# Kernel tuning notes

Hardware: AMD Instinct MI355X
Metric: run time of the kernel (lower is better)

Reference implementation:

```python
import jax, jax.numpy as jnp
import numpy as np

B, T, C, H, D = 2, 2048, 768, 12, 64
ATTN_MULT = 0.125  # 1/sqrt(head_dim)


def setup_inputs() -> dict:
    key = jax.random.key(0)
    k0, k1, k2 = jax.random.split(key, 3)
    x = jax.random.normal(k0, (B, T, C), jnp.float32)
    w_attn = jax.random.normal(k1, (3 * H * D, C), jnp.float32) * 0.02
    b_attn = jnp.zeros((3 * H * D,), jnp.float32)
    w_proj = jax.random.normal(k2, (C, H * D), jnp.float32) * 0.02
    b_proj = jnp.zeros((C,), jnp.float32)
    return {"x": x, "w_attn": w_attn, "b_attn": b_attn, "w_proj": w_proj, "b_proj": b_proj}


def reference(x, w_attn, b_attn, w_proj, b_proj):
    Bx, Tx, Cx = x.shape
    # fused qkv projection (torch nn.Linear: x @ W^T + b)
    qkv = x @ w_attn.T + b_attn                      # [B,T,3*H*D]
    q, k, v = jnp.split(qkv, 3, axis=2)
    def to_heads(t):
        return t.reshape(Bx, Tx, H, D).transpose(0, 2, 1, 3)  # [B,H,T,D]
    q, k, v = to_heads(q), to_heads(k), to_heads(v)
    att = jnp.einsum('bhqd,bhkd->bhqk', q, k) * ATTN_MULT     # [B,H,T,T]

    causal = jnp.tril(jnp.ones((Tx, Tx), dtype=bool))
    # selection scores from head 0 (selective attention)
    S = jax.nn.relu(att[:, 0])                                # [B,T,T]
    # prevent_from_masking_myself: zero diagonal; protect_bos_token: zero key col 0
    smask = causal & ~jnp.eye(Tx, dtype=bool)
    smask = smask.at[:, 0].set(False)
    S = jnp.where(smask, S, 0.0)
    # exclusive cumulative sum over the query dim: F[i,j] = sum_{i'<i} S[i',j]
    Fmask = jnp.cumsum(S, axis=-2) - S                        # [B,T,T]
    att = att - Fmask[:, None]                                # broadcast over heads

    att = jnp.where(causal, att, -jnp.inf)
    p = jax.nn.softmax(att, axis=-1)                          # [B,H,T,T]
    y = jnp.einsum('bhqk,bhkd->bhqd', p, v)                   # [B,H,T,D]
    y = y.transpose(0, 2, 1, 3).reshape(Bx, Tx, H * D)
    return y @ w_proj.T + b_proj
```

## Files before the change

### kernel.cpp

```cpp
#include <hip/hip_runtime.h>
#include <hip/hip_bf16.h>

#define BB 2
#define TT 2048
#define CC 768
#define HH 12
#define DD 64
#define NQKV 2304
#define MTOT (BB*TT)
#define CH 32
#define NCH (TT/CH)

typedef __bf16 bf16x8 __attribute__((ext_vector_type(8)));
typedef __bf16 bf16x4 __attribute__((ext_vector_type(4)));
typedef float  f32x4  __attribute__((ext_vector_type(4)));

__device__ __forceinline__ f32x4 mfma16(bf16x8 a, bf16x8 b, f32x4 c) {
    return __builtin_amdgcn_mfma_f32_16x16x32_bf16(a, b, c, 0, 0, 0);
}

__device__ __forceinline__ void load_lds16(const void* g, void* l) {
    __builtin_amdgcn_global_load_lds(
        (const __attribute__((address_space(1))) void*)g,
        (__attribute__((address_space(3))) void*)l, 16, 0, 0);
}

__global__ __launch_bounds__(256) void cvt_bf16_kernel(
    const float* __restrict__ x, const float* __restrict__ wa, const float* __restrict__ wp,
    __bf16* __restrict__ xb, __bf16* __restrict__ wab, __bf16* __restrict__ wpb)
{
    const long NX = (long)MTOT * CC;
    const long NWA = (long)NQKV * CC;
    long idx = ((long)blockIdx.x * 256 + threadIdx.x) * 4;
    const float* src; __bf16* dst; long off;
    if (idx < NX)            { src = x;  dst = xb;  off = idx; }
    else if (idx < NX + NWA) { src = wa; dst = wab; off = idx - NX; }
    else                     { src = wp; dst = wpb; off = idx - NX - NWA; }
    float4 v = *(const float4*)(src + off);
    bf16x4 o;
    o[0] = (__bf16)v.x; o[1] = (__bf16)v.y; o[2] = (__bf16)v.z; o[3] = (__bf16)v.w;
    *(bf16x4*)(dst + off) = o;
}

template<int EPI>
__global__ __launch_bounds__(256, 2) void gemm_nt_kernel(
    const __bf16* __restrict__ A, const __bf16* __restrict__ Bw,
    const float* __restrict__ bias,
    __bf16* __restrict__ oBF, float* __restrict__ oF32, int K)
{
    __shared__ __align__(16) __bf16 As[128 * 32];
    __shared__ __align__(16) __bf16 Bs[128 * 32];
    const int tid = threadIdx.x;
    const int m0 = blockIdx.y * 128, n0 = blockIdx.x * 128;
    const int w = tid >> 6, lane = tid & 63, quad = lane >> 4, l16 = lane & 15;
    const int wm = (w >> 1) * 64, wn = (w & 1) * 64;
    const int grow = w * 16 + (lane >> 2);
    const int gcol = (lane & 3) * 8;
    __bf16* AsW = As + w * 512;
    __bf16* BsW = Bs + w * 512;

    f32x4 acc[4][4] = {};

    for (int kt = 0; kt < K; kt += 32) {
        __syncthreads();
        load_lds16(A  + (long)(m0 + grow) * K + kt + gcol,      AsW);
        load_lds16(A  + (long)(m0 + grow + 64) * K + kt + gcol, AsW + 2048);
        load_lds16(Bw + (long)(n0 + grow) * K + kt + gcol,      BsW);
        load_lds16(Bw + (long)(n0 + grow + 64) * K + kt + gcol, BsW + 2048);
        __syncthreads();

        bf16x8 af[4], bfr[4];
#pragma unroll
        for (int g = 0; g < 4; g++)  af[g]  = *(const bf16x8*)(As + (wm + g * 16 + l16) * 32 + quad * 8);
#pragma unroll
        for (int jb = 0; jb < 4; jb++) bfr[jb] = *(const bf16x8*)(Bs + (wn + jb * 16 + l16) * 32 + quad * 8);
#pragma unroll
        for (int g = 0; g < 4; g++)
#pragma unroll
            for (int jb = 0; jb < 4; jb++)
                acc[g][jb] = mfma16(af[g], bfr[jb], acc[g][jb]);
    }

    const int ldc = (EPI == 0) ? NQKV : CC;
#pragma unroll
    for (int jb = 0; jb < 4; jb++) {
        const int n = n0 + wn + jb * 16 + l16;
        const float bv = bias[n];
#pragma unroll
        for (int g = 0; g < 4; g++) {
#pragma unroll
            for (int r = 0; r < 4; r++) {
                const int m = m0 + wm + g * 16 + quad * 4 + r;
                const float v = acc[g][jb][r] + bv;
                if (EPI == 0) oBF[(long)m * ldc + n] = (__bf16)v;
                else          oF32[(long)m * ldc + n] = v;
            }
        }
    }
}

__global__ __launch_bounds__(256) void transpose_v_kernel(
    const __bf16* __restrict__ qkv, __bf16* __restrict__ vT)
{
    __shared__ __bf16 Tl[64][72];
    const int tt = blockIdx.x, h = blockIdx.y, b = blockIdx.z;
    const int tid = threadIdx.x;
    const int r8 = tid >> 3, c8 = (tid & 7) * 8;
    const __bf16* src = qkv + (long)(b * TT + tt * 64) * NQKV + 1536 + h * 64;
#pragma unroll
    for (int p = 0; p < 2; p++) {
        const int row = p * 32 + r8;
        bf16x8 v = *(const bf16x8*)(src + (long)row * NQKV + c8);
#pragma unroll
        for (int e = 0; e < 8; e++) Tl[c8 + e][row] = v[e];
    }
    __syncthreads();
    __bf16* dst = vT + ((long)(b * HH + h) << 6) * TT + tt * 64;
#pragma unroll
    for (int p = 0; p < 2; p++) {
        const int d = p * 32 + r8;
        *(bf16x8*)(dst + (long)d * TT + c8) = *(const bf16x8*)(&Tl[d][c8]);
    }
}

__global__ __launch_bounds__(256) void sgemm_kernel(
    const __bf16* __restrict__ qkv, __bf16* __restrict__ S, float* __restrict__ csum)
{
    const int tj = blockIdx.x, ti = blockIdx.y, b = blockIdx.z;
    if (tj > ti) return;
    const int w = threadIdx.x >> 6, lane = threadIdx.x & 63, quad = lane >> 4, l16 = lane & 15;
    const int i0 = ti * 64 + w * 16;
    const int chunk = ti * 2 + (w >> 1);

    const __bf16* qp = qkv + (long)(b * TT + i0 + l16) * NQKV + quad * 8;
    bf16x8 a0 = *(const bf16x8*)qp, a1 = *(const bf16x8*)(qp + 32);
    const __bf16* kbase = qkv + (long)(b * TT) * NQKV + 768;

#pragma unroll
    for (int jb = 0; jb < 4; jb++) {
        const __bf16* kp = kbase + (long)(tj * 64 + jb * 16 + l16) * NQKV + quad * 8;
        bf16x8 b0 = *(const bf16x8*)kp, b1 = *(const bf16x8*)(kp + 32);
        f32x4 acc = {};
        acc = mfma16(a0, b0, acc);
        acc = mfma16(a1, b1, acc);
        const int j = tj * 64 + jb * 16 + l16;
        float colsum = 0.0f;
#pragma unroll
        for (int r = 0; r < 4; r++) {
            const int i = i0 + quad * 4 + r;
            float v = fmaxf(acc[r] * 0.125f, 0.0f);
            v = (j >= 1 && j < i) ? v : 0.0f;
            S[((long)b * TT + i) * TT + j] = (__bf16)v;
            colsum += v;
        }
        colsum += __shfl_xor(colsum, 16);
        colsum += __shfl_xor(colsum, 32);
        if (quad == 0)
            atomicAdd(&csum[((long)b * NCH + chunk) * TT + j], colsum);
    }
}

__global__ __launch_bounds__(256) void scan_write_kernel(
    const __bf16* __restrict__ S, const float* __restrict__ csum, __bf16* __restrict__ Fo)
{
    const int chunk = blockIdx.y, b = blockIdx.z;
    const int ib = chunk * CH;
    const int j0 = blockIdx.x * 256;
    if (j0 >= ib + CH) return;
    const int j = j0 + threadIdx.x;
    float off = 0.0f;
    for (int c = 0; c < chunk; c++) off += csum[((long)b * NCH + c) * TT + j];
    const __bf16* ps = S  + ((long)b * TT + ib) * TT + j;
    __bf16*       pf = Fo + ((long)b * TT + ib) * TT + j;
#pragma unroll
    for (int ii = 0; ii < CH; ii++) {
        float v = ((ib + ii) > j) ? (float)ps[(long)ii * TT] : 0.0f;
        pf[(long)ii * TT] = (__bf16)off;
        off += v;
    }
}

__global__ __launch_bounds__(128, 2) void flash_kernel(
    const __bf16* __restrict__ qkv, const __bf16* __restrict__ vT,
    const __bf16* __restrict__ F, __bf16* __restrict__ y)
{
    __shared__ __align__(16) __bf16 Ks[2][64 * 64];
    __shared__ __align__(16) __bf16 Vs[2][64 * 64];
    __shared__ __align__(16) __bf16 Pls[2][16 * 72];
    const int gid = blockIdx.x;
    const int xs = gid & 7, s = gid >> 3;
    const int gi = xs + ((s >> 5) << 3);
    const int bid = s & 31;
    const int h = gi % 12, b = gi / 12;
    const int w = threadIdx.x >> 6, lane = threadIdx.x & 63, quad = lane >> 4, l16 = lane & 15;
    const int rl = lane >> 3;
    const int cs8 = ((lane & 7) ^ rl) * 8;
    const int sw0 = ((quad)     ^ (l16 & 7)) * 8;
    const int sw1 = ((quad + 4) ^ (l16 & 7)) * 8;
    __bf16* Pl = &Pls[w][0];
    const __bf16* kb = qkv + (long)(b * TT) * NQKV + 768 + h * 64;
    const __bf16* vb = vT + ((long)(b * HH + h) << 6) * TT;
    const __bf16* Fbase = F + (long)b * TT * TT;

    const int qt0 = bid, qt1 = 63 - bid;
    const int n0 = (qt0 >> 1) + 1, n1 = (qt1 >> 1) + 1;
    const int N = n0 + n1;

    int i0 = qt0 * 32 + w * 16;
    const __bf16* qp = qkv + (long)(b * TT + i0 + l16) * NQKV + h * 64 + quad * 8;
    bf16x8 aq0 = *(const bf16x8*)qp;
    bf16x8 aq1 = *(const bf16x8*)(qp + 32);

    f32x4 O[4] = {};
    float lr[4] = {0.0f, 0.0f, 0.0f, 0.0f};
    __bf16 Fn[4][4];

    {
        __bf16* KsW = Ks[0] + w * 2048;
        __bf16* VsW = Vs[0] + w * 2048;
#pragma unroll
        for (int t = 0; t < 4; t++)
            load_lds16(kb + (long)(w * 32 + t * 8 + rl) * NQKV + cs8, KsW + t * 512);
#pragma unroll
        for (int t = 0; t < 4; t++)
            load_lds16(vb + (long)(w * 32 + t * 8 + rl) * TT + cs8, VsW + t * 512);
        const __bf16* Fb = Fbase + (long)i0 * TT;
#pragma unroll
        for (int jh = 0; jh < 4; jh++)
#pragma unroll
            for (int r = 0; r < 4; r++)
                Fn[jh][r] = Fb[(long)(quad * 4 + r) * TT + jh * 16 + l16];
    }

    for (int it = 0; it < N; it++) {
        const int ph = (it >= n0);
        const int jt = (it - (ph ? n0 : 0)) << 6;
        const int qt = ph ? qt1 : qt0;
        const int jtend = (qt >> 1) << 6;

        __syncthreads();

        __bf16 Fc[4][4];
#pragma unroll
        for (int jh = 0; jh < 4; jh++)
#pragma unroll
            for (int r = 0; r < 4; r++)
                Fc[jh][r] = Fn[jh][r];

        if (it + 1 < N) {
            const int ph2 = (it + 1 >= n0);
            const int jt2 = ((it + 1) - (ph2 ? n0 : 0)) << 6;
            __bf16* KsW = Ks[(it + 1) & 1] + w * 2048;
            __bf16* VsW = Vs[(it + 1) & 1] + w * 2048;
#pragma unroll
            for (int t = 0; t < 4; t++)
                load_lds16(kb + (long)(jt2 + w * 32 + t * 8 + rl) * NQKV + cs8, KsW + t * 512);
#pragma unroll
            for (int t = 0; t < 4; t++)
                load_lds16(vb + (long)(w * 32 + t * 8 + rl) * TT + jt2 + cs8, VsW + t * 512);
            const int i0n = (ph2 ? qt1 : qt0) * 32 + w * 16;
            const __bf16* Fb2 = Fbase + (long)i0n * TT;
#pragma unroll
            for (int jh = 0; jh < 4; jh++)
#pragma unroll
                for (int r = 0; r < 4; r++)
                    Fn[jh][r] = Fb2[(long)(quad * 4 + r) * TT + jt2 + jh * 16 + l16];
        }
        __builtin_amdgcn_sched_barrier(0);

        const __bf16* Kc = Ks[it & 1];
        const __bf16* Vc = Vs[it & 1];
        float sc[4][4];
#pragma unroll
        for (int jh = 0; jh < 4; jh++) {
            const int jr = jh * 16 + l16;
            const bf16x8 kc0 = *(const bf16x8*)(Kc + (jr << 6) + sw0);
            const bf16x8 kc1 = *(const bf16x8*)(Kc + (jr << 6) + sw1);
            f32x4 acc = {};
            acc = mfma16(aq0, kc0, acc);
            acc = mfma16(aq1, kc1, acc);
#pragma unroll
            for (int r = 0; r < 4; r++) sc[jh][r] = acc[r];
        }
        if (jt == jtend) {
#pragma unroll
            for (int jh = 0; jh < 4; jh++) {
                const int j = jt + jh * 16 + l16;
#pragma unroll
                for (int r = 0; r < 4; r++) {
                    const int i = i0 + quad * 4 + r;
                    float v = fmaf(sc[jh][r], 0.125f, -(float)Fc[jh][r]);
                    v = (j <= i) ? v : -35.0f;
                    const float p = __expf(v);
                    sc[jh][r] = p;
                    lr[r] += p;
                }
            }
        } else {
#pragma unroll
            for (int jh = 0; jh < 4; jh++) {
#pragma unroll
                for (int r = 0; r < 4; r++) {
                    float v = fmaf(sc[jh][r], 0.125f, -(float)Fc[jh][r]);
                    const float p = __expf(v);
                    sc[jh][r] = p;
                    lr[r] += p;
                }
            }
        }
#pragma unroll
        for (int r = 0; r < 4; r++) {
            const int il = quad * 4 + r;
#pragma unroll
            for (int jh = 0; jh < 4; jh++)
                Pl[il * 72 + jh * 16 + l16] = (__bf16)sc[jh][r];
        }
        const bf16x8 ap0 = *(const bf16x8*)(Pl + l16 * 72 + quad * 8);
        const bf16x8 ap1 = *(const bf16x8*)(Pl + l16 * 72 + 32 + quad * 8);
#pragma unroll
        for (int db = 0; db < 4; db++) {
            const bf16x8 vv0 = *(const bf16x8*)(Vc + ((db * 16 + l16) << 6) + sw0);
            const bf16x8 vv1 = *(const bf16x8*)(Vc + ((db * 16 + l16) << 6) + sw1);
            O[db] = mfma16(ap0, vv0, O[db]);
            O[db] = mfma16(ap1, vv1, O[db]);
        }
        if (jt == jtend) {
            float inv[4];
#pragma unroll
            for (int r = 0; r < 4; r++) {
                float s2 = lr[r];
#pragma unroll
                for (int off = 8; off >= 1; off >>= 1) s2 += __shfl_xor(s2, off, 16);
                inv[r] = 1.0f / s2;
            }
#pragma unroll
            for (int db = 0; db < 4; db++) {
#pragma unroll
                for (int r = 0; r < 4; r++) {
                    const int i = i0 + quad * 4 + r;
                    y[((long)(b * TT + i)) * (HH * DD) + h * 64 + db * 16 + l16] = (__bf16)(O[db][r] * inv[r]);
                }
            }
#pragma unroll
            for (int db = 0; db < 4; db++) { O[db][0] = 0.f; O[db][1] = 0.f; O[db][2] = 0.f; O[db][3] = 0.f; }
            lr[0] = lr[1] = lr[2] = lr[3] = 0.0f;
            if (!ph) {
                i0 = qt1 * 32 + w * 16;
                const __bf16* qp2 = qkv + (long)(b * TT + i0 + l16) * NQKV + h * 64 + quad * 8;
                aq0 = *(const bf16x8*)qp2;
                aq1 = *(const bf16x8*)(qp2 + 32);
            }
        }
    }
}

extern "C" void kernel_launch(void* const* d_in, const int* in_sizes, int n_in,
                              void* d_out, int out_size, void* d_ws, size_t ws_size,
                              hipStream_t stream)
{
    const float* x      = (const float*)d_in[0];
    const float* w_attn = (const float*)d_in[1];
    const float* b_attn = (const float*)d_in[2];
    const float* w_proj = (const float*)d_in[3];
    const float* b_proj = (const float*)d_in[4];
    float* out = (float*)d_out;

    char* ws = (char*)d_ws;
    __bf16* xb   = (__bf16*)ws; ws += (long)MTOT * CC * 2;
    __bf16* wab  = (__bf16*)ws; ws += (long)NQKV * CC * 2;
    __bf16* wpb  = (__bf16*)ws; ws += (long)CC * (HH*DD) * 2;
    __bf16* qkvb = (__bf16*)ws; ws += (long)MTOT * NQKV * 2;
    __bf16* vtb  = (__bf16*)ws; ws += (long)BB * HH * TT * DD * 2;
    __bf16* SF   = (__bf16*)ws; ws += (long)BB * TT * TT * 2;
    __bf16* Fo   = (__bf16*)ws; ws += (long)BB * TT * TT * 2;
    float*  cs   = (float*)ws;  ws += (long)BB * NCH * TT * 4;
    __bf16* yb   = (__bf16*)ws; ws += (long)MTOT * (HH*DD) * 2;

    hipMemsetAsync(cs, 0, (long)BB * NCH * TT * 4, stream);
    cvt_bf16_kernel<<<5376, 256, 0, stream>>>(x, w_attn, w_proj, xb, wab, wpb);
    gemm_nt_kernel<0><<<dim3(NQKV / 128, MTOT / 128), 256, 0, stream>>>(
        xb, wab, b_attn, qkvb, nullptr, CC);
    transpose_v_kernel<<<dim3(TT / 64, HH, BB), 256, 0, stream>>>(qkvb, vtb);
    sgemm_kernel<<<dim3(TT / 64, TT / 64, BB), 256, 0, stream>>>(qkvb, SF, cs);
    scan_write_kernel<<<dim3(TT / 256, NCH, BB), 256, 0, stream>>>(SF, cs, Fo);
    flash_kernel<<<dim3(768), 128, 0, stream>>>(qkvb, vtb, Fo, yb);
    gemm_nt_kernel<1><<<dim3(CC / 128, MTOT / 128), 256, 0, stream>>>(
        yb, wpb, b_proj, nullptr, out, HH * DD);
}
```

Baseline: 221.5 us.

## Fuse V transpose into QKV GEMM epilogue, memset into cvt, unpair flash tiles

The QKV GEMM epilogue now writes the V portion directly in transposed layout, removing the separate transpose kernel. Zeroing of the column-sum buffer moves into the conversion kernel, dropping the memset launch. The flash kernel now gives each block a single query tile in longest-first order across twice as many blocks, instead of pairing a short and a long tile per block. This cuts launches and a pass over V, in exchange for narrower strided V stores in the GEMM epilogue and a different load-balance pattern.

```diff
diff --git a/kernel.cpp b/kernel.cpp
--- a/kernel.cpp
+++ b/kernel.cpp
@@ -27,11 +27,19 @@
 
 __global__ __launch_bounds__(256) void cvt_bf16_kernel(
     const float* __restrict__ x, const float* __restrict__ wa, const float* __restrict__ wp,
-    __bf16* __restrict__ xb, __bf16* __restrict__ wab, __bf16* __restrict__ wpb)
+    __bf16* __restrict__ xb, __bf16* __restrict__ wab, __bf16* __restrict__ wpb,
+    float* __restrict__ cs)
 {
     const long NX = (long)MTOT * CC;
     const long NWA = (long)NQKV * CC;
+    const long NWP = (long)CC * (HH*DD);
+    const long NTOT = NX + NWA + NWP;
     long idx = ((long)blockIdx.x * 256 + threadIdx.x) * 4;
+    if (idx >= NTOT) {
+        float4 z = {0.f, 0.f, 0.f, 0.f};
+        *(float4*)(cs + (idx - NTOT)) = z;
+        return;
+    }
     const float* src; __bf16* dst; long off;
     if (idx < NX)            { src = x;  dst = xb;  off = idx; }
     else if (idx < NX + NWA) { src = wa; dst = wab; off = idx - NX; }
@@ -46,7 +54,8 @@
 __global__ __launch_bounds__(256, 2) void gemm_nt_kernel(
     const __bf16* __restrict__ A, const __bf16* __restrict__ Bw,
     const float* __restrict__ bias,
-    __bf16* __restrict__ oBF, float* __restrict__ oF32, int K)
+    __bf16* __restrict__ oQKV, __bf16* __restrict__ oVT,
+    float* __restrict__ oF32, int K)
 {
     __shared__ __align__(16) __bf16 As[128 * 32];
     __shared__ __align__(16) __bf16 Bs[128 * 32];
@@ -81,45 +90,41 @@
                 acc[g][jb] = mfma16(af[g], bfr[jb], acc[g][jb]);
     }
 
-    const int ldc = (EPI == 0) ? NQKV : CC;
 #pragma unroll
     for (int jb = 0; jb < 4; jb++) {
         const int n = n0 + wn + jb * 16 + l16;
         const float bv = bias[n];
-#pragma unroll
-        for (int g = 0; g < 4; g++) {
-#pragma unroll
-            for (int r = 0; r < 4; r++) {
-                const int m = m0 + wm + g * 16 + quad * 4 + r;
-                const float v = acc[g][jb][r] + bv;
-                if (EPI == 0) oBF[(long)m * ldc + n] = (__bf16)v;
-                else          oF32[(long)m * ldc + n] = v;
+        if (EPI == 1) {
+#pragma unroll
+            for (int g = 0; g < 4; g++)
+#pragma unroll
+                for (int r = 0; r < 4; r++) {
+                    const int m = m0 + wm + g * 16 + quad * 4 + r;
+                    oF32[(long)m * CC + n] = acc[g][jb][r] + bv;
+                }
+        } else {
+            const int which = n / 768;
+            if (which < 2) {
+#pragma unroll
+                for (int g = 0; g < 4; g++)
+#pragma unroll
+                    for (int r = 0; r < 4; r++) {
+                        const int m = m0 + wm + g * 16 + quad * 4 + r;
+                        oQKV[(long)m * NQKV + n] = (__bf16)(acc[g][jb][r] + bv);
+                    }
+            } else {
+                const int rem = n - 1536, hh = rem >> 6, d = rem & 63;
+#pragma unroll
+                for (int g = 0; g < 4; g++) {
+                    const int m = m0 + wm + g * 16 + quad * 4;
+                    const int b = m >> 11, t = m & 2047;
+                    bf16x4 pk;
+#pragma unroll
+                    for (int r = 0; r < 4; r++) pk[r] = (__bf16)(acc[g][jb][r] + bv);
+                    *(bf16x4*)(oVT + ((long)(((b * HH + hh) << 6) + d)) * TT + t) = pk;
+                }
             }
         }
-    }
-}
-
-__global__ __launch_bounds__(256) void transpose_v_kernel(
-    const __bf16* __restrict__ qkv, __bf16* __restrict__ vT)
-{
-    __shared__ __bf16 Tl[64][72];
-    const int tt = blockIdx.x, h = blockIdx.y, b = blockIdx.z;
-    const int tid = threadIdx.x;
-    const int r8 = tid >> 3, c8 = (tid & 7) * 8;
-    const __bf16* src = qkv + (long)(b * TT + tt * 64) * NQKV + 1536 + h * 64;
-#pragma unroll
-    for (int p = 0; p < 2; p++) {
-        const int row = p * 32 + r8;
-        bf16x8 v = *(const bf16x8*)(src + (long)row * NQKV + c8);
-#pragma unroll
-        for (int e = 0; e < 8; e++) Tl[c8 + e][row] = v[e];
-    }
-    __syncthreads();
-    __bf16* dst = vT + ((long)(b * HH + h) << 6) * TT + tt * 64;
-#pragma unroll
-    for (int p = 0; p < 2; p++) {
-        const int d = p * 32 + r8;
-        *(bf16x8*)(dst + (long)d * TT + c8) = *(const bf16x8*)(&Tl[d][c8]);
     }
 }
 
@@ -188,9 +193,9 @@
     __shared__ __align__(16) __bf16 Vs[2][64 * 64];
     __shared__ __align__(16) __bf16 Pls[2][16 * 72];
     const int gid = blockIdx.x;
-    const int xs = gid & 7, s = gid >> 3;
-    const int gi = xs + ((s >> 5) << 3);
-    const int bid = s & 31;
+    const int xs = gid & 7, r9 = gid >> 3;
+    const int qt = 63 - r9 / 3;
+    const int gi = xs + ((r9 % 3) << 3);
     const int h = gi % 12, b = gi / 12;
     const int w = threadIdx.x >> 6, lane = threadIdx.x & 63, quad = lane >> 4, l16 = lane & 15;
     const int rl = lane >> 3;
@@ -202,18 +207,16 @@
     const __bf16* vb = vT + ((long)(b * HH + h) << 6) * TT;
     const __bf16* Fbase = F + (long)b * TT * TT;
 
-    const int qt0 = bid, qt1 = 63 - bid;
-    const int n0 = (qt0 >> 1) + 1, n1 = (qt1 >> 1) + 1;
-    const int N = n0 + n1;
-
-    int i0 = qt0 * 32 + w * 16;
+    const int i0 = qt * 32 + w * 16;
     const __bf16* qp = qkv + (long)(b * TT + i0 + l16) * NQKV + h * 64 + quad * 8;
-    bf16x8 aq0 = *(const bf16x8*)qp;
-    bf16x8 aq1 = *(const bf16x8*)(qp + 32);
+    const bf16x8 aq0 = *(const bf16x8*)qp;
+    const bf16x8 aq1 = *(const bf16x8*)(qp + 32);
+    const __bf16* Fb = Fbase + (long)i0 * TT;
 
     f32x4 O[4] = {};
     float lr[4] = {0.0f, 0.0f, 0.0f, 0.0f};
     __bf16 Fn[4][4];
+    const int jtend = (qt >> 1) << 6;
 
     {
         __bf16* KsW = Ks[0] + w * 2048;
@@ -224,7 +227,6 @@
 #pragma unroll
         for (int t = 0; t < 4; t++)
             load_lds16(vb + (long)(w * 32 + t * 8 + rl) * TT + cs8, VsW + t * 512);
-        const __bf16* Fb = Fbase + (long)i0 * TT;
 #pragma unroll
         for (int jh = 0; jh < 4; jh++)
 #pragma unroll
@@ -232,12 +234,8 @@
                 Fn[jh][r] = Fb[(long)(quad * 4 + r) * TT + jh * 16 + l16];
     }
 
-    for (int it = 0; it < N; it++) {
-        const int ph = (it >= n0);
-        const int jt = (it - (ph ? n0 : 0)) << 6;
-        const int qt = ph ? qt1 : qt0;
-        const int jtend = (qt >> 1) << 6;
-
+    for (int jt = 0; jt <= jtend; jt += 64) {
+        const int buf = (jt >> 6) & 1;
         __syncthreads();
 
         __bf16 Fc[4][4];
@@ -247,29 +245,26 @@
             for (int r = 0; r < 4; r++)
                 Fc[jh][r] = Fn[jh][r];
 
-        if (it + 1 < N) {
-            const int ph2 = (it + 1 >= n0);
-            const int jt2 = ((it + 1) - (ph2 ? n0 : 0)) << 6;
-            __bf16* KsW = Ks[(it + 1) & 1] + w * 2048;
-            __bf16* VsW = Vs[(it + 1) & 1] + w * 2048;
+        if (jt + 64 <= jtend) {
+            const int jt2 = jt + 64;
+            __bf16* KsW = Ks[buf ^ 1] + w * 2048;
+            __bf16* VsW = Vs[buf ^ 1] + w * 2048;
 #pragma unroll
             for (int t = 0; t < 4; t++)
                 load_lds16(kb + (long)(jt2 + w * 32 + t * 8 + rl) * NQKV + cs8, KsW + t * 512);
 #pragma unroll
             for (int t = 0; t < 4; t++)
                 load_lds16(vb + (long)(w * 32 + t * 8 + rl) * TT + jt2 + cs8, VsW + t * 512);
-            const int i0n = (ph2 ? qt1 : qt0) * 32 + w * 16;
-            const __bf16* Fb2 = Fbase + (long)i0n * TT;
 #pragma unroll
             for (int jh = 0; jh < 4; jh++)
 #pragma unroll
                 for (int r = 0; r < 4; r++)
-                    Fn[jh][r] = Fb2[(long)(quad * 4 + r) * TT + jt2 + jh * 16 + l16];
+                    Fn[jh][r] = Fb[(long)(quad * 4 + r) * TT + jt2 + jh * 16 + l16];
         }
         __builtin_amdgcn_sched_barrier(0);
 
-        const __bf16* Kc = Ks[it & 1];
-        const __bf16* Vc = Vs[it & 1];
+        const __bf16* Kc = Ks[buf];
+        const __bf16* Vc = Vs[buf];
         float sc[4][4];
 #pragma unroll
         for (int jh = 0; jh < 4; jh++) {
@@ -324,32 +319,22 @@
             O[db] = mfma16(ap0, vv0, O[db]);
             O[db] = mfma16(ap1, vv1, O[db]);
         }
-        if (jt == jtend) {
-            float inv[4];
-#pragma unroll
-            for (int r = 0; r < 4; r++) {
-                float s2 = lr[r];
-#pragma unroll
-                for (int off = 8; off >= 1; off >>= 1) s2 += __shfl_xor(s2, off, 16);
-                inv[r] = 1.0f / s2;
-            }
-#pragma unroll
-            for (int db = 0; db < 4; db++) {
-#pragma unroll
-                for (int r = 0; r < 4; r++) {
-                    const int i = i0 + quad * 4 + r;
-                    y[((long)(b * TT + i)) * (HH * DD) + h * 64 + db * 16 + l16] = (__bf16)(O[db][r] * inv[r]);
-                }
-            }
-#pragma unroll
-            for (int db = 0; db < 4; db++) { O[db][0] = 0.f; O[db][1] = 0.f; O[db][2] = 0.f; O[db][3] = 0.f; }
-            lr[0] = lr[1] = lr[2] = lr[3] = 0.0f;
-            if (!ph) {
-                i0 = qt1 * 32 + w * 16;
-                const __bf16* qp2 = qkv + (long)(b * TT + i0 + l16) * NQKV + h * 64 + quad * 8;
-                aq0 = *(const bf16x8*)qp2;
-                aq1 = *(const bf16x8*)(qp2 + 32);
-            }
+    }
+
+    float inv[4];
+#pragma unroll
+    for (int r = 0; r < 4; r++) {
+        float s2 = lr[r];
+#pragma unroll
+        for (int off = 8; off >= 1; off >>= 1) s2 += __shfl_xor(s2, off, 16);
+        inv[r] = 1.0f / s2;
+    }
+#pragma unroll
+    for (int db = 0; db < 4; db++) {
+#pragma unroll
+        for (int r = 0; r < 4; r++) {
+            const int i = i0 + quad * 4 + r;
+            y[((long)(b * TT + i)) * (HH * DD) + h * 64 + db * 16 + l16] = (__bf16)(O[db][r] * inv[r]);
         }
     }
 }
@@ -376,14 +361,12 @@
     float*  cs   = (float*)ws;  ws += (long)BB * NCH * TT * 4;
     __bf16* yb   = (__bf16*)ws; ws += (long)MTOT * (HH*DD) * 2;
 
-    hipMemsetAsync(cs, 0, (long)BB * NCH * TT * 4, stream);
-    cvt_bf16_kernel<<<5376, 256, 0, stream>>>(x, w_attn, w_proj, xb, wab, wpb);
+    cvt_bf16_kernel<<<5376 + 256, 256, 0, stream>>>(x, w_attn, w_proj, xb, wab, wpb, cs);
     gemm_nt_kernel<0><<<dim3(NQKV / 128, MTOT / 128), 256, 0, stream>>>(
-        xb, wab, b_attn, qkvb, nullptr, CC);
-    transpose_v_kernel<<<dim3(TT / 64, HH, BB), 256, 0, stream>>>(qkvb, vtb);
+        xb, wab, b_attn, qkvb, vtb, nullptr, CC);
     sgemm_kernel<<<dim3(TT / 64, TT / 64, BB), 256, 0, stream>>>(qkvb, SF, cs);
     scan_write_kernel<<<dim3(TT / 256, NCH, BB), 256, 0, stream>>>(SF, cs, Fo);
-    flash_kernel<<<dim3(768), 128, 0, stream>>>(qkvb, vtb, Fo, yb);
+    flash_kernel<<<dim3(1536), 128, 0, stream>>>(qkvb, vtb, Fo, yb);
     gemm_nt_kernel<1><<<dim3(CC / 128, MTOT / 128), 256, 0, stream>>>(
-        yb, wpb, b_proj, nullptr, out, HH * DD);
-}
+        yb, wpb, b_proj, nullptr, nullptr, out, HH * DD);
+}
```

After: 208.2 us. 1.06x faster.
